# Optimization experiments

Hardware: AMD Instinct MI355X
Metric: run time of the kernel (lower is better)

## Reference

```python
import jax, jax.numpy as jnp
import numpy as np

DIM = 768
NUM_HEADS = 12
HEAD_DIM = DIM // NUM_HEADS  # 64
H = W = 64                   # input_size


def get_rel_pos(q_size, k_size, rel_pos):
    # q_size == k_size and rel_pos has 2*size-1 rows, so no interpolation needed.
    coords = jnp.arange(q_size)[:, None] - jnp.arange(k_size)[None, :] + (k_size - 1)
    return rel_pos[coords]  # (q_size, k_size, head_dim)


def add_decomposed_rel_pos(attn, q, rel_pos_h, rel_pos_w, q_size, k_size):
    q_h, q_w = q_size
    k_h, k_w = k_size
    Rh = get_rel_pos(q_h, k_h, rel_pos_h)  # (q_h, k_h, c)
    Rw = get_rel_pos(q_w, k_w, rel_pos_w)  # (q_w, k_w, c)
    Bn, _, c = q.shape
    r_q = q.reshape(Bn, q_h, q_w, c)
    rel_h = jnp.einsum('bhwc,hkc->bhwk', r_q, Rh)  # (Bn, q_h, q_w, k_h)
    rel_w = jnp.einsum('bhwc,wkc->bhwk', r_q, Rw)  # (Bn, q_h, q_w, k_w)
    attn = attn.reshape(Bn, q_h, q_w, k_h, k_w)
    attn = attn + rel_h[..., :, None] + rel_w[..., None, :]
    return attn.reshape(Bn, q_h * q_w, k_h * k_w)


def setup_inputs() -> dict:
    key = jax.random.key(0)
    ks = jax.random.split(key, 7)
    inv = 1.0 / np.sqrt(DIM)
    return {
        'x': jax.random.normal(ks[0], (1, H, W, DIM), jnp.float32),
        'w_qkv': jax.random.normal(ks[1], (DIM, 3 * DIM), jnp.float32) * inv,
        'b_qkv': jax.random.normal(ks[2], (3 * DIM,), jnp.float32) * 0.02,
        'w_proj': jax.random.normal(ks[3], (DIM, DIM), jnp.float32) * inv,
        'b_proj': jax.random.normal(ks[4], (DIM,), jnp.float32) * 0.02,
        'rel_pos_h': jax.random.normal(ks[5], (2 * H - 1, HEAD_DIM), jnp.float32) * 0.02,
        'rel_pos_w': jax.random.normal(ks[6], (2 * W - 1, HEAD_DIM), jnp.float32) * 0.02,
    }


def reference(x, w_qkv, b_qkv, w_proj, b_proj, rel_pos_h, rel_pos_w):
    B, h, w, _ = x.shape
    N = h * w
    scale = HEAD_DIM ** (-0.5)
    qkv = x @ w_qkv + b_qkv                                   # (B, H, W, 3*dim)
    qkv = qkv.reshape(B, N, 3, NUM_HEADS, HEAD_DIM)
    qkv = jnp.transpose(qkv, (2, 0, 3, 1, 4)).reshape(3, B * NUM_HEADS, N, HEAD_DIM)
    q, k, v = qkv[0], qkv[1], qkv[2]
    attn = jnp.einsum('bnd,bmd->bnm', q * scale, k)           # (B*nh, N, N)
    attn = add_decomposed_rel_pos(attn, q, rel_pos_h, rel_pos_w, (h, w), (h, w))
    attn = jax.nn.softmax(attn.astype(jnp.float32), axis=-1).astype(q.dtype)
    out = attn @ v                                            # (B*nh, N, hd)
    out = out.reshape(B, NUM_HEADS, h, w, HEAD_DIM)
    out = jnp.transpose(out, (0, 2, 3, 1, 4)).reshape(B, h, w, DIM)
    return out @ w_proj + b_proj
```

## Files before the change

kernel.cpp:

```cpp
#include <hip/hip_runtime.h>
#include <math.h>

#define N_TOK 4096
#define DIM   768
#define NH    12
#define HD    64

typedef __attribute__((ext_vector_type(8))) short bf16x8;
typedef __attribute__((ext_vector_type(4))) float f32x4;
typedef __attribute__((ext_vector_type(4))) unsigned short us4;

__device__ inline unsigned short f2b(float f) {
    union { float f; unsigned int u; } v; v.f = f;
    unsigned int r = v.u + 0x7FFFu + ((v.u >> 16) & 1u);
    return (unsigned short)(r >> 16);
}
__device__ inline float b2f(unsigned short u) {
    union { unsigned int u; float f; } v; v.u = ((unsigned int)u) << 16;
    return v.f;
}
__device__ inline unsigned int pk2(float lo, float hi) {
    unsigned int u;
    asm("v_cvt_pk_bf16_f32 %0, %1, %2" : "=v"(u) : "v"(lo), "v"(hi));
    return u;
}
__device__ inline void gload16(const void* g, void* l) {
    __builtin_amdgcn_global_load_lds(
        (const __attribute__((address_space(1))) unsigned int*)g,
        (__attribute__((address_space(3))) unsigned int*)l, 16, 0, 0);
}

__global__ __launch_bounds__(256)
void conv_split(const float* __restrict__ X, unsigned short* __restrict__ hi,
                unsigned short* __restrict__ lo, int n4) {
    int i = blockIdx.x * 256 + threadIdx.x;
    int stride = gridDim.x * 256;
    for (; i < n4; i += stride) {
        float4 v = ((const float4*)X)[i];
        us4 h, l;
        h.x = f2b(v.x); l.x = f2b(v.x - b2f(h.x));
        h.y = f2b(v.y); l.y = f2b(v.y - b2f(h.y));
        h.z = f2b(v.z); l.z = f2b(v.z - b2f(h.z));
        h.w = f2b(v.w); l.w = f2b(v.w - b2f(h.w));
        ((us4*)hi)[i] = h;
        ((us4*)lo)[i] = l;
    }
}

__global__ __launch_bounds__(256)
void transpose_split(const float* __restrict__ W, unsigned short* __restrict__ Thi,
                     unsigned short* __restrict__ Tlo, int K, int N) {
    __shared__ float tile[64][65];
    const int t = threadIdx.x;
    const int k0 = blockIdx.y * 64, n0 = blockIdx.x * 64;
#pragma unroll
    for (int u = 0; u < 4; ++u) {
        int idx = u * 256 + t;
        int r = idx >> 4, c4 = idx & 15;
        float4 v = *(const float4*)&W[(size_t)(k0 + r) * N + n0 + c4 * 4];
        tile[r][c4 * 4 + 0] = v.x; tile[r][c4 * 4 + 1] = v.y;
        tile[r][c4 * 4 + 2] = v.z; tile[r][c4 * 4 + 3] = v.w;
    }
    __syncthreads();
#pragma unroll
    for (int u = 0; u < 4; ++u) {
        int idx = u * 256 + t;
        int col = idx >> 4, c4 = idx & 15;
        float a0 = tile[c4 * 4 + 0][col], a1 = tile[c4 * 4 + 1][col];
        float a2 = tile[c4 * 4 + 2][col], a3 = tile[c4 * 4 + 3][col];
        us4 h, l;
        h.x = f2b(a0); l.x = f2b(a0 - b2f(h.x));
        h.y = f2b(a1); l.y = f2b(a1 - b2f(h.y));
        h.z = f2b(a2); l.z = f2b(a2 - b2f(h.z));
        h.w = f2b(a3); l.w = f2b(a3 - b2f(h.w));
        size_t o = (size_t)(n0 + col) * K + k0 + c4 * 4;
        *(us4*)&Thi[o] = h;
        *(us4*)&Tlo[o] = l;
    }
}

template<int M, int N, int K, int MODE>
__global__ __launch_bounds__(256)
void gemm_split(const unsigned short* __restrict__ Ahi, const unsigned short* __restrict__ Alo,
                const unsigned short* __restrict__ BThi, const unsigned short* __restrict__ BTlo,
                const float* __restrict__ bias, float* __restrict__ Cout,
                unsigned short* __restrict__ qkvbf) {
    __shared__ __align__(16) char smem[28672];
    const int t = threadIdx.x, lane = t & 63, w = t >> 6;
    const int c15 = lane & 15, g = lane >> 4;
    const int nwg = gridDim.x * gridDim.y;
    int lin = blockIdx.y * gridDim.x + blockIdx.x;
    lin = (lin & 7) * (nwg >> 3) + (lin >> 3);
    const int m0 = (lin / gridDim.x) * 128, n0 = (lin % gridDim.x) * 96;
    const int wm = (w >> 1) * 64, wn = (w & 1) * 48;

    f32x4 acc[4][3];
#pragma unroll
    for (int i = 0; i < 4; ++i)
#pragma unroll
        for (int j = 0; j < 3; ++j) acc[i][j] = f32x4{0.f, 0.f, 0.f, 0.f};

    for (int k0 = 0; k0 < K; k0 += 32) {
        __syncthreads();
#pragma unroll
        for (int p = 0; p < 2; ++p) {
            int off = p * 4096 + w * 1024 + lane * 16;
            int row = off >> 6;
            int gs  = ((off >> 4) & 3) ^ (row & 3);
            size_t ae = (size_t)(m0 + row) * K + k0 + gs * 8;
            char* dstA = smem + off - lane * 16;
            gload16(Ahi + ae, dstA);
            gload16(Alo + ae, dstA + 8192);
            if (off < 6144) {
                size_t be = (size_t)(n0 + row) * K + k0 + gs * 8;
                char* dstB = smem + 16384 + off - lane * 16;
                gload16(BThi + be, dstB);
                gload16(BTlo + be, dstB + 6144);
            }
        }
        __syncthreads();

        bf16x8 ah[4], al[4], bh[3], bl[3];
#pragma unroll
        for (int i = 0; i < 4; ++i) {
            int ra = wm + i * 16 + c15;
            int boa = ra * 64 + ((g ^ (ra & 3)) << 4);
            ah[i] = *(const bf16x8*)(smem + boa);
            al[i] = *(const bf16x8*)(smem + 8192 + boa);
        }
#pragma unroll
        for (int j = 0; j < 3; ++j) {
            int rb = wn + j * 16 + c15;
            int bob = rb * 64 + ((g ^ (rb & 3)) << 4);
            bh[j] = *(const bf16x8*)(smem + 16384 + bob);
            bl[j] = *(const bf16x8*)(smem + 22528 + bob);
        }
        __builtin_amdgcn_s_setprio(1);
#pragma unroll
        for (int i = 0; i < 4; ++i)
#pragma unroll
            for (int j = 0; j < 3; ++j) {
                acc[i][j] = __builtin_amdgcn_mfma_f32_16x16x32_bf16(ah[i], bh[j], acc[i][j], 0, 0, 0);
                acc[i][j] = __builtin_amdgcn_mfma_f32_16x16x32_bf16(ah[i], bl[j], acc[i][j], 0, 0, 0);
                acc[i][j] = __builtin_amdgcn_mfma_f32_16x16x32_bf16(al[i], bh[j], acc[i][j], 0, 0, 0);
            }
        __builtin_amdgcn_s_setprio(0);
    }

    const int nq = n0 + wn;
    if (MODE == 0) {
#pragma unroll
        for (int j = 0; j < 3; ++j) {
            float bb = bias[nq + j * 16 + c15];
#pragma unroll
            for (int i = 0; i < 4; ++i)
#pragma unroll
                for (int r = 0; r < 4; ++r) {
                    int mm = m0 + wm + i * 16 + g * 4 + r;
                    Cout[(size_t)mm * N + nq + j * 16 + c15] = acc[i][j][r] + bb;
                }
        }
    } else {
        const int which = nq / 768;
        const float scale = (which == 0) ? 0.18033688f : 1.0f;
#pragma unroll
        for (int j = 0; j < 3; ++j) {
            int colg = nq + j * 16;
            int head = (colg % 768) >> 6;
            int dbase = colg & 63;
            float bb = bias[colg + c15];
#pragma unroll
            for (int i = 0; i < 4; ++i)
#pragma unroll
                for (int r = 0; r < 4; ++r) {
                    int mm = m0 + wm + i * 16 + g * 4 + r;
                    float val = acc[i][j][r] + bb;
                    qkvbf[((size_t)(which * NH + head) * N_TOK + mm) * 64 + dbase + c15] =
                        f2b(val * scale);
                }
        }
    }
}

__global__ __launch_bounds__(256)
void relpos_rw(const unsigned short* __restrict__ qkvbf,
               const float* __restrict__ rel_pos_w,
               unsigned short* __restrict__ rw) {
    const int qh = blockIdx.x;
    const int h  = blockIdx.y;
    const int t  = threadIdx.x, tx = t & 15, ty = t >> 4;
    const unsigned short* qbf = qkvbf + (size_t)h * N_TOK * 64;

    __shared__ float Qt[64][68];
    __shared__ float RW[127][68];

#pragma unroll
    for (int u = 0; u < 2; ++u) {
        int idx = u * 256 + t;
        int row = idx >> 3, ch = idx & 7;
        bf16x8 v = *(const bf16x8*)&qbf[(size_t)(qh * 64 + row) * 64 + ch * 8];
#pragma unroll
        for (int j = 0; j < 8; ++j)
            Qt[row][ch * 8 + j] = b2f((unsigned short)v[j]) * 8.0f;
    }
#pragma unroll
    for (int u = 0; u < 8; ++u) {
        int idx = u * 256 + t;
        if (idx < 127 * 16) {
            int row = idx >> 4, c4 = idx & 15;
            *(float4*)&RW[row][c4 * 4] =
                *(const float4*)&rel_pos_w[(size_t)row * HD + c4 * 4];
        }
    }
    __syncthreads();

    float acc2[4][4];
#pragma unroll
    for (int i = 0; i < 4; ++i)
#pragma unroll
        for (int j = 0; j < 4; ++j) acc2[i][j] = 0.f;

    for (int c4 = 0; c4 < 16; ++c4) {
        float4 q4[4];
#pragma unroll
        for (int i = 0; i < 4; ++i) q4[i] = *(float4*)&Qt[ty * 4 + i][c4 * 4];
#pragma unroll
        for (int i = 0; i < 4; ++i)
#pragma unroll
            for (int j = 0; j < 4; ++j) {
                float4 w4 = *(float4*)&RW[(ty * 4 + i) - (tx * 4 + j) + 63][c4 * 4];
                acc2[i][j] = fmaf(q4[i].x, w4.x, acc2[i][j]);
                acc2[i][j] = fmaf(q4[i].y, w4.y, acc2[i][j]);
                acc2[i][j] = fmaf(q4[i].z, w4.z, acc2[i][j]);
                acc2[i][j] = fmaf(q4[i].w, w4.w, acc2[i][j]);
            }
    }
#pragma unroll
    for (int i = 0; i < 4; ++i) {
        size_t base = ((size_t)h * N_TOK + qh * 64 + ty * 4 + i) * 64 + tx * 4;
        us4 w4;
        w4.x = f2b(acc2[i][0]); w4.y = f2b(acc2[i][1]);
        w4.z = f2b(acc2[i][2]); w4.w = f2b(acc2[i][3]);
        *(us4*)&rw[base] = w4;
    }
}

__global__ __launch_bounds__(256, 3)
void attn_mfma(const unsigned short* __restrict__ qkvbf,
               const unsigned short* __restrict__ rw,
               const float* __restrict__ rel_pos_h,
               unsigned short* __restrict__ aohi, unsigned short* __restrict__ aolo) {
    int lin = blockIdx.y * 64 + blockIdx.x;
    lin = (lin & 7) * 96 + (lin >> 3);
    const int qt = lin & 63, h = lin >> 6;
    const int t = threadIdx.x;
    const int lane = t & 63, w = t >> 6;
    const int c15 = lane & 15, g = lane >> 4;

    const unsigned short* qbf = qkvbf + ((size_t)(0 * NH + h)) * N_TOK * 64;
    const unsigned short* kbf = qkvbf + ((size_t)(1 * NH + h)) * N_TOK * 64;
    const unsigned short* vbf = qkvbf + ((size_t)(2 * NH + h)) * N_TOK * 64;

    __shared__ __align__(16) unsigned short Qs[64 * 64];
    __shared__ __align__(16) unsigned short Ks[2][64 * 64];
    __shared__ __align__(16) unsigned short Vt[2][80 * 64];
    __shared__ __align__(16) unsigned short Ps[4][16 * 64];

    const int pi = t & 31;
    const int d0 = (t >> 5) * 8;
    const int vm = (pi & 15) + (pi >> 4) * 32;
    const int pbase = (pi & 15) * 4 + (pi >> 4) * 2;
    const int kr_row = t >> 3, kr_ch = t & 7;
    bf16x8 kr0, kr1, vr0, vr1;
    auto LOADKV = [&](int kt) {
        kr0 = *(const bf16x8*)&kbf[(size_t)(kt * 64 + kr_row) * 64 + kr_ch * 8];
        kr1 = *(const bf16x8*)&kbf[(size_t)(kt * 64 + 32 + kr_row) * 64 + kr_ch * 8];
        vr0 = *(const bf16x8*)&vbf[(size_t)(kt * 64 + vm) * 64 + d0];
        vr1 = *(const bf16x8*)&vbf[(size_t)(kt * 64 + vm + 16) * 64 + d0];
    };
    auto WRITEKV = [&](int buf) {
        int b0 = (kr_ch * 16) ^ ((kr_row & 7) << 4);
        *(bf16x8*)((char*)&Ks[buf][kr_row * 64] + b0) = kr0;
        int r1 = 32 + kr_row;
        int b1 = (kr_ch * 16) ^ ((r1 & 7) << 4);
        *(bf16x8*)((char*)&Ks[buf][r1 * 64] + b1) = kr1;
#pragma unroll
        for (int j = 0; j < 8; ++j) {
            int d = d0 + j;
            unsigned int pk = (unsigned int)(unsigned short)vr0[j]
                            | ((unsigned int)(unsigned short)vr1[j] << 16);
            int boff = (pbase * 2) ^ ((d & 7) << 4);
            *(unsigned int*)((char*)&Vt[buf][d * 64] + boff) = pk;
        }
    };

#pragma unroll
    for (int u = 0; u < 2; ++u) {
        int idx = u * 256 + t;
        int row = idx >> 3, ch = idx & 7;
        bf16x8 v = *(const bf16x8*)&qbf[(size_t)(qt * 64 + row) * 64 + ch * 8];
        int boff = (ch * 16) ^ ((row & 7) << 4);
        *(bf16x8*)((char*)&Qs[row * 64] + boff) = v;
    }
#pragma unroll
    for (int u = 0; u < 4; ++u) {
        int idx = u * 256 + t;
        int row = idx >> 4, c4 = idx & 15;
        float4 v = *(const float4*)&rel_pos_h[(size_t)(qt - row + 63) * HD + c4 * 4];
        us4 p = {f2b(v.x * 8.f), f2b(v.y * 8.f), f2b(v.z * 8.f), f2b(v.w * 8.f)};
        int boff = (c4 * 8) ^ ((row & 7) << 4);
        *(us4*)((char*)&Ks[1][row * 64] + boff) = p;
    }
#pragma unroll
    for (int u = 0; u < 4; ++u) {
        int idx = u * 256 + t;
        int dr = 64 + (idx >> 6), pos = idx & 63;
        unsigned short val = (dr == 64) ? (unsigned short)0x3F80 : (unsigned short)0;
        int boff = (pos * 2) ^ ((dr & 7) << 4);
        *(unsigned short*)((char*)&Vt[0][dr * 64] + boff) = val;
        *(unsigned short*)((char*)&Vt[1][dr * 64] + boff) = val;
    }
    LOADKV(0);
    __syncthreads();

    WRITEKV(0);
    bf16x8 qf[2];
    {
        int row = w * 16 + c15;
#pragma unroll
        for (int ks = 0; ks < 2; ++ks) {
            int boff = (ks * 64 + g * 16) ^ ((row & 7) << 4);
            qf[ks] = *(bf16x8*)((char*)&Qs[row * 64] + boff);
        }
    }
    f32x4 rhacc[4];
#pragma unroll
    for (int nt = 0; nt < 4; ++nt) {
        int krow = nt * 16 + c15;
        int b0 = (g * 16) ^ ((krow & 7) << 4);
        int b1 = (64 + g * 16) ^ ((krow & 7) << 4);
        bf16x8 rf0 = *(bf16x8*)((char*)&Ks[1][krow * 64] + b0);
        bf16x8 rf1 = *(bf16x8*)((char*)&Ks[1][krow * 64] + b1);
        f32x4 z = {0.f, 0.f, 0.f, 0.f};
        z = __builtin_amdgcn_mfma_f32_16x16x32_bf16(qf[0], rf0, z, 0, 0, 0);
        z = __builtin_amdgcn_mfma_f32_16x16x32_bf16(qf[1], rf1, z, 0, 0, 0);
        rhacc[nt] = z;
    }
    LOADKV(1);

    float rwm[4][4];
#pragma unroll
    for (int nt = 0; nt < 4; ++nt)
#pragma unroll
        for (int r = 0; r < 4; ++r)
            rwm[nt][r] = b2f(rw[((size_t)h * N_TOK + qt * 64 + w * 16 + g * 4 + r) * 64
                               + nt * 16 + c15]);

    f32x4 acc[5];
#pragma unroll
    for (int nt = 0; nt < 5; ++nt) acc[nt] = f32x4{0.f, 0.f, 0.f, 0.f};

    __syncthreads();

#pragma unroll
    for (int kt4 = 0; kt4 < 4; ++kt4) {
#pragma unroll 2
        for (int kti = 0; kti < 16; ++kti) {
            const int kt = kt4 * 16 + kti;
            const int cur = kt & 1, nxt = cur ^ 1;
            if (kt < 63) WRITEKV(nxt);
            if (kt < 62) LOADKV(kt + 2);

            f32x4 s[4];
            __builtin_amdgcn_s_setprio(1);
#pragma unroll
            for (int nt = 0; nt < 4; ++nt) {
                int krow = nt * 16 + c15;
                int b0 = (g * 16) ^ ((krow & 7) << 4);
                int b1 = (64 + g * 16) ^ ((krow & 7) << 4);
                bf16x8 kf0 = *(bf16x8*)((char*)&Ks[cur][krow * 64] + b0);
                bf16x8 kf1 = *(bf16x8*)((char*)&Ks[cur][krow * 64] + b1);
                f32x4 z = {0.f, 0.f, 0.f, 0.f};
                z = __builtin_amdgcn_mfma_f32_16x16x32_bf16(qf[0], kf0, z, 0, 0, 0);
                z = __builtin_amdgcn_mfma_f32_16x16x32_bf16(qf[1], kf1, z, 0, 0, 0);
                s[nt] = z;
            }
            __builtin_amdgcn_s_setprio(0);

            float rhv[4];
#pragma unroll
            for (int r = 0; r < 4; ++r)
                rhv[r] = __shfl(rhacc[kt4][r], (lane & 48) | kti, 64);
#pragma unroll
            for (int nt = 0; nt < 4; ++nt)
#pragma unroll
                for (int r = 0; r < 4; ++r)
                    s[nt][r] += rhv[r] + rwm[nt][r];

            float mx[4];
#pragma unroll
            for (int r = 0; r < 4; ++r)
                mx[r] = fmaxf(fmaxf(s[0][r], s[1][r]), fmaxf(s[2][r], s[3][r]));
#pragma unroll
            for (int off = 1; off < 16; off <<= 1)
#pragma unroll
                for (int r = 0; r < 4; ++r)
                    mx[r] = fmaxf(mx[r], __shfl_xor(mx[r], off, 64));

            bool need = false;
#pragma unroll
            for (int r = 0; r < 4; ++r) need |= (mx[r] > 11.5f);
            if (__any(need ? 1 : 0)) {
#pragma unroll
                for (int r = 0; r < 4; ++r) {
                    float delta = fmaxf(mx[r], 0.f);
                    float corr = __builtin_amdgcn_exp2f(-delta);
#pragma unroll
                    for (int nt = 0; nt < 5; ++nt) acc[nt][r] *= corr;
#pragma unroll
                    for (int nt = 0; nt < 4; ++nt) {
                        rwm[nt][r] -= delta;
                        s[nt][r]   -= delta;
                    }
                }
            }
#pragma unroll
            for (int nt = 0; nt < 4; ++nt)
#pragma unroll
                for (int r = 0; r < 4; ++r)
                    s[nt][r] = __builtin_amdgcn_exp2f(s[nt][r]);

#pragma unroll
            for (int r = 0; r < 4; ++r) {
                int row = g * 4 + r;
                int hr = (row ^ (row >> 1)) & 7;
                uint2 pv;
                pv.x = pk2(s[0][r], s[1][r]);
                pv.y = pk2(s[2][r], s[3][r]);
                int boff = (c15 * 8) ^ (hr << 4);
                *(uint2*)((char*)&Ps[w][row * 64] + boff) = pv;
            }

            const int hc = (c15 ^ (c15 >> 1)) & 7;
            __builtin_amdgcn_s_setprio(1);
#pragma unroll
            for (int ks = 0; ks < 2; ++ks) {
                int pb = (g * 32 + ks * 16) ^ (hc << 4);
                bf16x8 pf = *(bf16x8*)((char*)&Ps[w][c15 * 64] + pb);
#pragma unroll
                for (int nt = 0; nt < 4; ++nt) {
                    int drow = nt * 16 + c15;
                    int vb = (g * 32 + ks * 16) ^ ((drow & 7) << 4);
                    bf16x8 vf = *(bf16x8*)((char*)&Vt[cur][drow * 64] + vb);
                    acc[nt] = __builtin_amdgcn_mfma_f32_16x16x32_bf16(pf, vf, acc[nt], 0, 0, 0);
                }
                int drow5 = 64 + c15;
                int vb5 = (g * 32 + ks * 16) ^ ((drow5 & 7) << 4);
                bf16x8 vf5 = *(bf16x8*)((char*)&Vt[cur][drow5 * 64] + vb5);
                acc[4] = __builtin_amdgcn_mfma_f32_16x16x32_bf16(pf, vf5, acc[4], 0, 0, 0);
            }
            __builtin_amdgcn_s_setprio(0);

            __syncthreads();
        }
    }

#pragma unroll
    for (int r = 0; r < 4; ++r) {
        float l = __shfl(acc[4][r], lane & 48, 64);
        float inv = 1.0f / l;
        size_t orow = (size_t)(qt * 64 + w * 16 + g * 4 + r) * 768 + h * HD;
#pragma unroll
        for (int nt = 0; nt < 4; ++nt) {
            float o = acc[nt][r] * inv;
            unsigned short hi = f2b(o);
            unsigned short lo = f2b(o - b2f(hi));
            aohi[orow + nt * 16 + c15] = hi;
            aolo[orow + nt * 16 + c15] = lo;
        }
    }
}

extern "C" void kernel_launch(void* const* d_in, const int* in_sizes, int n_in,
                              void* d_out, int out_size, void* d_ws, size_t ws_size,
                              hipStream_t stream) {
    const float* x      = (const float*)d_in[0];
    const float* w_qkv  = (const float*)d_in[1];
    const float* b_qkv  = (const float*)d_in[2];
    const float* w_proj = (const float*)d_in[3];
    const float* b_proj = (const float*)d_in[4];
    const float* rph    = (const float*)d_in[5];
    const float* rpw    = (const float*)d_in[6];
    float* out = (float*)d_out;

    char* p = (char*)d_ws;
    unsigned short* qkvbf = (unsigned short*)p; p += (size_t)3 * NH * N_TOK * 64 * 2;
    unsigned short* rwbf  = (unsigned short*)p; p += (size_t)NH * N_TOK * 64 * 2;
    unsigned short* xhi   = (unsigned short*)p; p += (size_t)N_TOK * 768 * 2;
    unsigned short* xlo   = (unsigned short*)p; p += (size_t)N_TOK * 768 * 2;
    unsigned short* wqThi = (unsigned short*)p; p += (size_t)2304 * 768 * 2;
    unsigned short* wqTlo = (unsigned short*)p; p += (size_t)2304 * 768 * 2;
    unsigned short* wpThi = (unsigned short*)p; p += (size_t)768 * 768 * 2;
    unsigned short* wpTlo = (unsigned short*)p; p += (size_t)768 * 768 * 2;
    unsigned short* aohi = xhi;
    unsigned short* aolo = xlo;

    conv_split<<<1024, 256, 0, stream>>>(x, xhi, xlo, N_TOK * 768 / 4);
    transpose_split<<<dim3(36, 12), 256, 0, stream>>>(w_qkv, wqThi, wqTlo, 768, 2304);
    transpose_split<<<dim3(12, 12), 256, 0, stream>>>(w_proj, wpThi, wpTlo, 768, 768);

    gemm_split<N_TOK, 2304, 768, 1><<<dim3(24, 32), 256, 0, stream>>>(
        xhi, xlo, wqThi, wqTlo, b_qkv, nullptr, qkvbf);

    relpos_rw<<<dim3(64, NH), 256, 0, stream>>>(qkvbf, rpw, rwbf);

    attn_mfma<<<dim3(64, NH), 256, 0, stream>>>(qkvbf, rwbf, rph, aohi, aolo);

    gemm_split<N_TOK, 768, 768, 0><<<dim3(8, 32), 256, 0, stream>>>(
        aohi, aolo, wpThi, wpTlo, b_proj, out, nullptr);
}
```

Before: 301.8 us.

## Transpose attention MFMAs to keep P in registers via shuffles instead of LDS

Swaps MFMA operand order so S is computed transposed (keys on rows, queries on columns). This makes each query's max reduction mostly lane-local, and lets the P operand for the PV MFMA be built with register shuffles instead of a per-wave LDS round trip. The row-sum column previously packed into V is replaced by a separate ones-vector MFMA. The rel-h bias is moved into a shared LDS table, and the output is staged through LDS for vectorized bf16x8 stores. It adds many shuffles per tile and bf16 rounding of the rel-h term, in exchange for removing the Ps LDS writes and reads and the padded V rows.

```diff
diff --git a/kernel.cpp b/kernel.cpp
--- a/kernel.cpp
+++ b/kernel.cpp
@@ -263,20 +263,18 @@
 
     __shared__ __align__(16) unsigned short Qs[64 * 64];
     __shared__ __align__(16) unsigned short Ks[2][64 * 64];
-    __shared__ __align__(16) unsigned short Vt[2][80 * 64];
-    __shared__ __align__(16) unsigned short Ps[4][16 * 64];
+    __shared__ __align__(16) unsigned short Vt[2][64 * 64];
+    __shared__ __align__(16) unsigned short RHs[64 * 64];
 
     const int pi = t & 31;
     const int d0 = (t >> 5) * 8;
-    const int vm = (pi & 15) + (pi >> 4) * 32;
-    const int pbase = (pi & 15) * 4 + (pi >> 4) * 2;
     const int kr_row = t >> 3, kr_ch = t & 7;
     bf16x8 kr0, kr1, vr0, vr1;
     auto LOADKV = [&](int kt) {
         kr0 = *(const bf16x8*)&kbf[(size_t)(kt * 64 + kr_row) * 64 + kr_ch * 8];
         kr1 = *(const bf16x8*)&kbf[(size_t)(kt * 64 + 32 + kr_row) * 64 + kr_ch * 8];
-        vr0 = *(const bf16x8*)&vbf[(size_t)(kt * 64 + vm) * 64 + d0];
-        vr1 = *(const bf16x8*)&vbf[(size_t)(kt * 64 + vm + 16) * 64 + d0];
+        vr0 = *(const bf16x8*)&vbf[(size_t)(kt * 64 + pi * 2) * 64 + d0];
+        vr1 = *(const bf16x8*)&vbf[(size_t)(kt * 64 + pi * 2 + 1) * 64 + d0];
     };
     auto WRITEKV = [&](int buf) {
         int b0 = (kr_ch * 16) ^ ((kr_row & 7) << 4);
@@ -289,7 +287,7 @@
             int d = d0 + j;
             unsigned int pk = (unsigned int)(unsigned short)vr0[j]
                             | ((unsigned int)(unsigned short)vr1[j] << 16);
-            int boff = (pbase * 2) ^ ((d & 7) << 4);
+            int boff = (pi * 4) ^ ((d & 7) << 4);
             *(unsigned int*)((char*)&Vt[buf][d * 64] + boff) = pk;
         }
     };
@@ -311,15 +309,6 @@
         int boff = (c4 * 8) ^ ((row & 7) << 4);
         *(us4*)((char*)&Ks[1][row * 64] + boff) = p;
     }
-#pragma unroll
-    for (int u = 0; u < 4; ++u) {
-        int idx = u * 256 + t;
-        int dr = 64 + (idx >> 6), pos = idx & 63;
-        unsigned short val = (dr == 64) ? (unsigned short)0x3F80 : (unsigned short)0;
-        int boff = (pos * 2) ^ ((dr & 7) << 4);
-        *(unsigned short*)((char*)&Vt[0][dr * 64] + boff) = val;
-        *(unsigned short*)((char*)&Vt[1][dr * 64] + boff) = val;
-    }
     LOADKV(0);
     __syncthreads();
 
@@ -328,156 +317,180 @@
     {
         int row = w * 16 + c15;
 #pragma unroll
-        for (int ks = 0; ks < 2; ++ks) {
-            int boff = (ks * 64 + g * 16) ^ ((row & 7) << 4);
-            qf[ks] = *(bf16x8*)((char*)&Qs[row * 64] + boff);
-        }
-    }
-    f32x4 rhacc[4];
-#pragma unroll
-    for (int nt = 0; nt < 4; ++nt) {
-        int krow = nt * 16 + c15;
-        int b0 = (g * 16) ^ ((krow & 7) << 4);
-        int b1 = (64 + g * 16) ^ ((krow & 7) << 4);
-        bf16x8 rf0 = *(bf16x8*)((char*)&Ks[1][krow * 64] + b0);
-        bf16x8 rf1 = *(bf16x8*)((char*)&Ks[1][krow * 64] + b1);
-        f32x4 z = {0.f, 0.f, 0.f, 0.f};
-        z = __builtin_amdgcn_mfma_f32_16x16x32_bf16(qf[0], rf0, z, 0, 0, 0);
-        z = __builtin_amdgcn_mfma_f32_16x16x32_bf16(qf[1], rf1, z, 0, 0, 0);
-        rhacc[nt] = z;
+        for (int ck = 0; ck < 2; ++ck) {
+            int boff = (ck * 64 + g * 16) ^ ((row & 7) << 4);
+            qf[ck] = *(bf16x8*)((char*)&Qs[row * 64] + boff);
+        }
+    }
+    {
+#pragma unroll
+        for (int nt = 0; nt < 4; ++nt) {
+            int krow = nt * 16 + c15;
+            int b0 = (g * 16) ^ ((krow & 7) << 4);
+            int b1 = (64 + g * 16) ^ ((krow & 7) << 4);
+            bf16x8 rf0 = *(bf16x8*)((char*)&Ks[1][krow * 64] + b0);
+            bf16x8 rf1 = *(bf16x8*)((char*)&Ks[1][krow * 64] + b1);
+            f32x4 z = {0.f, 0.f, 0.f, 0.f};
+            z = __builtin_amdgcn_mfma_f32_16x16x32_bf16(rf0, qf[0], z, 0, 0, 0);
+            z = __builtin_amdgcn_mfma_f32_16x16x32_bf16(rf1, qf[1], z, 0, 0, 0);
+#pragma unroll
+            for (int r = 0; r < 4; ++r)
+                RHs[(nt * 16 + g * 4 + r) * 64 + w * 16 + c15] = f2b(z[r]);
+        }
     }
     LOADKV(1);
 
+    const int qrow = qt * 64 + w * 16 + c15;
     float rwm[4][4];
 #pragma unroll
     for (int nt = 0; nt < 4; ++nt)
 #pragma unroll
         for (int r = 0; r < 4; ++r)
-            rwm[nt][r] = b2f(rw[((size_t)h * N_TOK + qt * 64 + w * 16 + g * 4 + r) * 64
-                               + nt * 16 + c15]);
-
-    f32x4 acc[5];
-#pragma unroll
-    for (int nt = 0; nt < 5; ++nt) acc[nt] = f32x4{0.f, 0.f, 0.f, 0.f};
+            rwm[nt][r] = b2f(rw[((size_t)h * N_TOK + qrow) * 64 + nt * 16 + g * 4 + r]);
+
+    f32x4 acc[4];
+    f32x4 acc5;
+#pragma unroll
+    for (int nt = 0; nt < 4; ++nt) acc[nt] = f32x4{0.f, 0.f, 0.f, 0.f};
+    acc5 = f32x4{0.f, 0.f, 0.f, 0.f};
+
+    union { unsigned int w4[4]; bf16x8 b; } onesu;
+    {
+        unsigned int ov = (c15 == 0) ? 0x3F803F80u : 0u;
+        onesu.w4[0] = ov; onesu.w4[1] = ov; onesu.w4[2] = ov; onesu.w4[3] = ov;
+    }
+    const int srcE = ((g & 1) << 5) + c15;
+    const int srcO = srcE + 16;
+    const bool hiSel = (g & 2) != 0;
 
     __syncthreads();
 
-#pragma unroll
-    for (int kt4 = 0; kt4 < 4; ++kt4) {
 #pragma unroll 2
-        for (int kti = 0; kti < 16; ++kti) {
-            const int kt = kt4 * 16 + kti;
-            const int cur = kt & 1, nxt = cur ^ 1;
-            if (kt < 63) WRITEKV(nxt);
-            if (kt < 62) LOADKV(kt + 2);
-
-            f32x4 s[4];
-            __builtin_amdgcn_s_setprio(1);
+    for (int kt = 0; kt < 64; ++kt) {
+        const int cur = kt & 1, nxt = cur ^ 1;
+        if (kt < 63) WRITEKV(nxt);
+        if (kt < 62) LOADKV(kt + 2);
+
+        f32x4 s[4];
+        __builtin_amdgcn_s_setprio(1);
+#pragma unroll
+        for (int nt = 0; nt < 4; ++nt) {
+            int krow = nt * 16 + c15;
+            int b0 = (g * 16) ^ ((krow & 7) << 4);
+            int b1 = (64 + g * 16) ^ ((krow & 7) << 4);
+            bf16x8 kf0 = *(bf16x8*)((char*)&Ks[cur][krow * 64] + b0);
+            bf16x8 kf1 = *(bf16x8*)((char*)&Ks[cur][krow * 64] + b1);
+            f32x4 z = {0.f, 0.f, 0.f, 0.f};
+            z = __builtin_amdgcn_mfma_f32_16x16x32_bf16(kf0, qf[0], z, 0, 0, 0);
+            z = __builtin_amdgcn_mfma_f32_16x16x32_bf16(kf1, qf[1], z, 0, 0, 0);
+            s[nt] = z;
+        }
+        __builtin_amdgcn_s_setprio(0);
+
+        float rhv = b2f(RHs[kt * 64 + w * 16 + c15]);
+#pragma unroll
+        for (int nt = 0; nt < 4; ++nt)
+#pragma unroll
+            for (int r = 0; r < 4; ++r)
+                s[nt][r] += rhv + rwm[nt][r];
+
+        float mx = s[0][0];
+#pragma unroll
+        for (int nt = 0; nt < 4; ++nt)
+#pragma unroll
+            for (int r = 0; r < 4; ++r) mx = fmaxf(mx, s[nt][r]);
+        if (__any(mx > 11.5f)) {
+            float rm = fmaxf(mx, __shfl_xor(mx, 16, 64));
+            rm = fmaxf(rm, __shfl_xor(rm, 32, 64));
+            float delta = fmaxf(rm, 0.f);
+            float corr = __builtin_amdgcn_exp2f(-delta);
 #pragma unroll
             for (int nt = 0; nt < 4; ++nt) {
-                int krow = nt * 16 + c15;
-                int b0 = (g * 16) ^ ((krow & 7) << 4);
-                int b1 = (64 + g * 16) ^ ((krow & 7) << 4);
-                bf16x8 kf0 = *(bf16x8*)((char*)&Ks[cur][krow * 64] + b0);
-                bf16x8 kf1 = *(bf16x8*)((char*)&Ks[cur][krow * 64] + b1);
-                f32x4 z = {0.f, 0.f, 0.f, 0.f};
-                z = __builtin_amdgcn_mfma_f32_16x16x32_bf16(qf[0], kf0, z, 0, 0, 0);
-                z = __builtin_amdgcn_mfma_f32_16x16x32_bf16(qf[1], kf1, z, 0, 0, 0);
-                s[nt] = z;
-            }
-            __builtin_amdgcn_s_setprio(0);
-
-            float rhv[4];
-#pragma unroll
-            for (int r = 0; r < 4; ++r)
-                rhv[r] = __shfl(rhacc[kt4][r], (lane & 48) | kti, 64);
-#pragma unroll
-            for (int nt = 0; nt < 4; ++nt)
-#pragma unroll
-                for (int r = 0; r < 4; ++r)
-                    s[nt][r] += rhv[r] + rwm[nt][r];
-
-            float mx[4];
-#pragma unroll
-            for (int r = 0; r < 4; ++r)
-                mx[r] = fmaxf(fmaxf(s[0][r], s[1][r]), fmaxf(s[2][r], s[3][r]));
-#pragma unroll
-            for (int off = 1; off < 16; off <<= 1)
-#pragma unroll
-                for (int r = 0; r < 4; ++r)
-                    mx[r] = fmaxf(mx[r], __shfl_xor(mx[r], off, 64));
-
-            bool need = false;
-#pragma unroll
-            for (int r = 0; r < 4; ++r) need |= (mx[r] > 11.5f);
-            if (__any(need ? 1 : 0)) {
 #pragma unroll
                 for (int r = 0; r < 4; ++r) {
-                    float delta = fmaxf(mx[r], 0.f);
-                    float corr = __builtin_amdgcn_exp2f(-delta);
-#pragma unroll
-                    for (int nt = 0; nt < 5; ++nt) acc[nt][r] *= corr;
-#pragma unroll
-                    for (int nt = 0; nt < 4; ++nt) {
-                        rwm[nt][r] -= delta;
-                        s[nt][r]   -= delta;
-                    }
+                    acc[nt][r] *= corr;
+                    rwm[nt][r] -= delta;
+                    s[nt][r]   -= delta;
                 }
             }
 #pragma unroll
-            for (int nt = 0; nt < 4; ++nt)
-#pragma unroll
-                for (int r = 0; r < 4; ++r)
-                    s[nt][r] = __builtin_amdgcn_exp2f(s[nt][r]);
-
-#pragma unroll
-            for (int r = 0; r < 4; ++r) {
-                int row = g * 4 + r;
-                int hr = (row ^ (row >> 1)) & 7;
-                uint2 pv;
-                pv.x = pk2(s[0][r], s[1][r]);
-                pv.y = pk2(s[2][r], s[3][r]);
-                int boff = (c15 * 8) ^ (hr << 4);
-                *(uint2*)((char*)&Ps[w][row * 64] + boff) = pv;
+            for (int r = 0; r < 4; ++r) acc5[r] *= corr;
+        }
+#pragma unroll
+        for (int nt = 0; nt < 4; ++nt)
+#pragma unroll
+            for (int r = 0; r < 4; ++r)
+                s[nt][r] = __builtin_amdgcn_exp2f(s[nt][r]);
+
+        unsigned int u0[2], u1[2], u2[2], u3[2];
+        u0[0] = pk2(s[0][0], s[0][1]); u0[1] = pk2(s[0][2], s[0][3]);
+        u1[0] = pk2(s[1][0], s[1][1]); u1[1] = pk2(s[1][2], s[1][3]);
+        u2[0] = pk2(s[2][0], s[2][1]); u2[1] = pk2(s[2][2], s[2][3]);
+        u3[0] = pk2(s[3][0], s[3][1]); u3[1] = pk2(s[3][2], s[3][3]);
+
+        __builtin_amdgcn_s_setprio(1);
+#pragma unroll
+        for (int ks = 0; ks < 2; ++ks) {
+            unsigned int a0, a1;
+            union { unsigned int w4[4]; bf16x8 b; } pu;
+            if (ks == 0) {
+                a0 = __shfl((int)u0[0], srcE); a1 = __shfl((int)u1[0], srcE);
+                pu.w4[0] = hiSel ? a1 : a0;
+                a0 = __shfl((int)u0[1], srcE); a1 = __shfl((int)u1[1], srcE);
+                pu.w4[1] = hiSel ? a1 : a0;
+                a0 = __shfl((int)u0[0], srcO); a1 = __shfl((int)u1[0], srcO);
+                pu.w4[2] = hiSel ? a1 : a0;
+                a0 = __shfl((int)u0[1], srcO); a1 = __shfl((int)u1[1], srcO);
+                pu.w4[3] = hiSel ? a1 : a0;
+            } else {
+                a0 = __shfl((int)u2[0], srcE); a1 = __shfl((int)u3[0], srcE);
+                pu.w4[0] = hiSel ? a1 : a0;
+                a0 = __shfl((int)u2[1], srcE); a1 = __shfl((int)u3[1], srcE);
+                pu.w4[1] = hiSel ? a1 : a0;
+                a0 = __shfl((int)u2[0], srcO); a1 = __shfl((int)u3[0], srcO);
+                pu.w4[2] = hiSel ? a1 : a0;
+                a0 = __shfl((int)u2[1], srcO); a1 = __shfl((int)u3[1], srcO);
+                pu.w4[3] = hiSel ? a1 : a0;
             }
-
-            const int hc = (c15 ^ (c15 >> 1)) & 7;
-            __builtin_amdgcn_s_setprio(1);
-#pragma unroll
-            for (int ks = 0; ks < 2; ++ks) {
-                int pb = (g * 32 + ks * 16) ^ (hc << 4);
-                bf16x8 pf = *(bf16x8*)((char*)&Ps[w][c15 * 64] + pb);
-#pragma unroll
-                for (int nt = 0; nt < 4; ++nt) {
-                    int drow = nt * 16 + c15;
-                    int vb = (g * 32 + ks * 16) ^ ((drow & 7) << 4);
-                    bf16x8 vf = *(bf16x8*)((char*)&Vt[cur][drow * 64] + vb);
-                    acc[nt] = __builtin_amdgcn_mfma_f32_16x16x32_bf16(pf, vf, acc[nt], 0, 0, 0);
-                }
-                int drow5 = 64 + c15;
-                int vb5 = (g * 32 + ks * 16) ^ ((drow5 & 7) << 4);
-                bf16x8 vf5 = *(bf16x8*)((char*)&Vt[cur][drow5 * 64] + vb5);
-                acc[4] = __builtin_amdgcn_mfma_f32_16x16x32_bf16(pf, vf5, acc[4], 0, 0, 0);
+            bf16x8 pf = pu.b;
+#pragma unroll
+            for (int nt = 0; nt < 4; ++nt) {
+                int drow = nt * 16 + c15;
+                int vb = (ks * 64 + g * 16) ^ ((drow & 7) << 4);
+                bf16x8 vf = *(bf16x8*)((char*)&Vt[cur][drow * 64] + vb);
+                acc[nt] = __builtin_amdgcn_mfma_f32_16x16x32_bf16(vf, pf, acc[nt], 0, 0, 0);
             }
-            __builtin_amdgcn_s_setprio(0);
-
-            __syncthreads();
-        }
-    }
-
-#pragma unroll
-    for (int r = 0; r < 4; ++r) {
-        float l = __shfl(acc[4][r], lane & 48, 64);
-        float inv = 1.0f / l;
-        size_t orow = (size_t)(qt * 64 + w * 16 + g * 4 + r) * 768 + h * HD;
-#pragma unroll
-        for (int nt = 0; nt < 4; ++nt) {
-            float o = acc[nt][r] * inv;
-            unsigned short hi = f2b(o);
-            unsigned short lo = f2b(o - b2f(hi));
-            aohi[orow + nt * 16 + c15] = hi;
-            aolo[orow + nt * 16 + c15] = lo;
-        }
+            acc5 = __builtin_amdgcn_mfma_f32_16x16x32_bf16(onesu.b, pf, acc5, 0, 0, 0);
+        }
+        __builtin_amdgcn_s_setprio(0);
+
+        __syncthreads();
+    }
+
+    float l = __shfl(acc5[0], c15, 64);
+    float inv = 1.0f / l;
+    float* T = (float*)&Ks[0][0];
+#pragma unroll
+    for (int nt = 0; nt < 4; ++nt)
+#pragma unroll
+        for (int r = 0; r < 4; ++r)
+            T[(nt * 16 + g * 4 + r) * 64 + w * 16 + c15] = acc[nt][r] * inv;
+    __syncthreads();
+
+    {
+        int q = t >> 2, ck = t & 3;
+        unsigned short hi[16], lo[16];
+#pragma unroll
+        for (int j = 0; j < 16; ++j) {
+            float o = T[(ck * 16 + j) * 64 + q];
+            hi[j] = f2b(o);
+            lo[j] = f2b(o - b2f(hi[j]));
+        }
+        size_t go = (size_t)(qt * 64 + q) * 768 + h * HD + ck * 16;
+        *(bf16x8*)&aohi[go]     = *(bf16x8*)&hi[0];
+        *(bf16x8*)&aohi[go + 8] = *(bf16x8*)&hi[8];
+        *(bf16x8*)&aolo[go]     = *(bf16x8*)&lo[0];
+        *(bf16x8*)&aolo[go + 8] = *(bf16x8*)&lo[8];
     }
 }
 
```

Measured after the change: 290.4 us. 1.04x faster.
